# Optimization experiments

Measured on AMD Instinct MI355X. Metric: run time of the kernel, lower is better.

Reference implementation:

```python
import jax, jax.numpy as jnp
import numpy as np

K, D, N, T, B = 8, 16, 32, 200, 2048
_LOG2PI = float(np.log(2.0 * np.pi))


def setup_inputs() -> dict:
    key = jax.random.key(0)
    ks = jax.random.split(key, 13)
    return {
        "discrete_states": jax.random.randint(ks[0], (B, T), 0, K),
        "continuous_states": jax.random.normal(ks[1], (B, T, D), dtype=jnp.float32),
        "obs": jax.random.normal(ks[2], (B, T, N), dtype=jnp.float32),
        "discrete_init_logits": jax.random.normal(ks[3], (K,), dtype=jnp.float32),
        "continuous_init_locs": jax.random.normal(ks[4], (K, D), dtype=jnp.float32),
        "continuous_init_log_scales": jax.random.normal(ks[5], (K, D), dtype=jnp.float32),
        "state_transition_logits": jax.random.normal(ks[6], (K, K), dtype=jnp.float32),
        "dynamics_matrices": jax.random.normal(ks[7], (K, D, D), dtype=jnp.float32) * 0.3,
        "dynamics_offsets": jax.random.normal(ks[8], (K, D), dtype=jnp.float32),
        # NOTE: original code uses dynamics_log_scales directly as a scale (missing .exp());
        # we keep that math faithfully but init it strictly positive to stay finite.
        "dynamics_log_scales": jax.random.uniform(ks[9], (K, D), minval=0.5, maxval=1.5, dtype=jnp.float32),
        "emission_matrices": jax.random.normal(ks[10], (K, N, D), dtype=jnp.float32),
        "emission_offsets": jax.random.normal(ks[11], (K, N), dtype=jnp.float32),
        "emission_log_scales": jax.random.normal(ks[12], (K, N), dtype=jnp.float32),
    }


def _normal_lp(x, loc, scale):
    # elementwise Normal log-prob
    return -0.5 * jnp.square((x - loc) / scale) - jnp.log(scale) - 0.5 * _LOG2PI


def reference(discrete_states, continuous_states, obs,
              discrete_init_logits, continuous_init_locs, continuous_init_log_scales,
              state_transition_logits, dynamics_matrices, dynamics_offsets,
              dynamics_log_scales, emission_matrices, emission_offsets,
              emission_log_scales):
    """log p(s_{1:T}, z_{1:T}, x_{1:T}) -> [B]"""
    s0 = discrete_states[:, 0]                      # [B]
    z0 = continuous_states[:, 0]                    # [B,D]
    # p(s_1)
    lp = jax.nn.log_softmax(discrete_init_logits)[s0]
    # p(z_1 | s_1)
    lp = lp + _normal_lp(z0, continuous_init_locs[s0],
                         jnp.exp(continuous_init_log_scales[s0])).sum(-1)
    # p(s_t | s_{t-1}) for t=2..T, fully vectorized over time
    s_prev = discrete_states[:, :-1]
    s_cur = discrete_states[:, 1:]
    trans = jax.nn.log_softmax(state_transition_logits, axis=-1)  # [K,K]
    lp = lp + trans[s_prev, s_cur].sum(-1)
    # p(z_t | z_{t-1}, s_t)
    A = dynamics_matrices[s_cur]                    # [B,T-1,D,D] gather
    dyn_loc = jnp.einsum('btij,btj->bti', A, continuous_states[:, :-1]) + dynamics_offsets[s_cur]
    dyn_scale = dynamics_log_scales[s_cur]          # faithful: original omits .exp()
    lp = lp + _normal_lp(continuous_states[:, 1:], dyn_loc, dyn_scale).sum((-1, -2))
    # p(x_t | z_t, s_t) for all t
    C = emission_matrices[discrete_states]          # [B,T,N,D] gather
    em_loc = jnp.einsum('btij,btj->bti', C, continuous_states) + emission_offsets[discrete_states]
    em_scale = jnp.exp(emission_log_scales[discrete_states])
    lp = lp + _normal_lp(obs, em_loc, em_scale).sum((-1, -2))
    return lp
```

## Files before the change

### kernel.cpp

```cpp
#include <hip/hip_runtime.h>

#define KK 8
#define DD 16
#define NN 32
#define TT 200
#define BB 2048

#define SCU 260
#define SAU 132
#define SE 36
#define SD 20

__device__ __forceinline__ float bflo(unsigned u) { return __uint_as_float(u << 16); }
__device__ __forceinline__ float bfhi(unsigned u) { return __uint_as_float(u & 0xffff0000u); }

__device__ __forceinline__ unsigned bfr(float f) {
  unsigned u = __float_as_uint(f);
  return (u + 0x7fffu + ((u >> 16) & 1u)) >> 16;
}
__device__ __forceinline__ unsigned bfpack(float f0, float f1) {
  return bfr(f0) | (bfr(f1) << 16);
}

__device__ __forceinline__ float dot16bf(const unsigned* __restrict__ row,
                                         const float* __restrict__ z) {
  uint4 w0 = *reinterpret_cast<const uint4*>(row);
  uint4 w1 = *reinterpret_cast<const uint4*>(row + 4);
  float a = bflo(w0.x) * z[0], b = bfhi(w0.x) * z[1];
  a = fmaf(bflo(w0.y), z[2], a);  b = fmaf(bfhi(w0.y), z[3], b);
  a = fmaf(bflo(w0.z), z[4], a);  b = fmaf(bfhi(w0.z), z[5], b);
  a = fmaf(bflo(w0.w), z[6], a);  b = fmaf(bfhi(w0.w), z[7], b);
  a = fmaf(bflo(w1.x), z[8], a);  b = fmaf(bfhi(w1.x), z[9], b);
  a = fmaf(bflo(w1.y), z[10], a); b = fmaf(bfhi(w1.y), z[11], b);
  a = fmaf(bflo(w1.z), z[12], a); b = fmaf(bfhi(w1.z), z[13], b);
  a = fmaf(bflo(w1.w), z[14], a); b = fmaf(bfhi(w1.w), z[15], b);
  return a + b;
}

__global__ __launch_bounds__(256) void slds_lp_kernel(
    const int* __restrict__ dsts,
    const float* __restrict__ zg,
    const float* __restrict__ obsg,
    const float* __restrict__ initlg,
    const float* __restrict__ initloc,
    const float* __restrict__ initls,
    const float* __restrict__ transg,
    const float* __restrict__ Ag,
    const float* __restrict__ dynoff,
    const float* __restrict__ dynls,
    const float* __restrict__ Cg,
    const float* __restrict__ emoff,
    const float* __restrict__ emls,
    float* __restrict__ out)
{
  __shared__ __align__(16) unsigned sCu[KK * SCU];
  __shared__ __align__(16) unsigned sAu[KK * SAU];
  __shared__ __align__(16) float sEmOff[KK * SE];
  __shared__ __align__(16) float sEmInv[KK * SE];
  __shared__ __align__(16) float sDynOff[KK * SD];
  __shared__ __align__(16) float sDynInv[KK * SD];
  __shared__ __align__(16) float sInitLoc[KK * SD];
  __shared__ __align__(16) float sInitInv[KK * SD];
  __shared__ float sTrans[KK * KK];
  __shared__ float sEmConst[KK];
  __shared__ float sDynConst[KK];
  __shared__ float sInitLp[KK];

  const float HALF_LOG2PI = 0.91893853320467274178f;
  const int tid = threadIdx.x;

  for (int i = tid; i < KK * NN * DD / 2; i += 256) {
    int k = i >> 8, r = i & 255;
    sCu[k * SCU + r] = bfpack(Cg[2 * i], Cg[2 * i + 1]);
  }
  for (int i = tid; i < KK * DD * DD / 2; i += 256) {
    int k = i >> 7, r = i & 127;
    sAu[k * SAU + r] = bfpack(Ag[2 * i], Ag[2 * i + 1]);
  }
  if (tid < KK * NN) {
    int k = tid >> 5, n = tid & 31;
    sEmOff[k * SE + n] = emoff[tid];
    sEmInv[k * SE + n] = expf(-emls[tid]);
  }
  if (tid < KK * DD) {
    int k = tid >> 4, d = tid & 15;
    sDynOff[k * SD + d] = dynoff[tid];
    sDynInv[k * SD + d] = 1.0f / dynls[tid];
    sInitLoc[k * SD + d] = initloc[tid];
    sInitInv[k * SD + d] = expf(-initls[tid]);
  }
  if (tid < KK * KK) {
    int kr = tid >> 3;
    float mx = transg[kr * KK];
    for (int j = 1; j < KK; ++j) mx = fmaxf(mx, transg[kr * KK + j]);
    float ss = 0.f;
    for (int j = 0; j < KK; ++j) ss += expf(transg[kr * KK + j] - mx);
    sTrans[tid] = transg[tid] - (logf(ss) + mx);
  }
  if (tid < KK) {
    int k = tid;
    float se = 0.f;
    for (int n = 0; n < NN; ++n) se -= emls[k * NN + n];
    sEmConst[k] = se - NN * HALF_LOG2PI;
    float sd = 0.f;
    for (int d = 0; d < DD; ++d) sd -= logf(dynls[k * DD + d]);
    sDynConst[k] = sd - DD * HALF_LOG2PI;
    float mx = initlg[0];
    for (int j = 1; j < KK; ++j) mx = fmaxf(mx, initlg[j]);
    float ss = 0.f;
    for (int j = 0; j < KK; ++j) ss += expf(initlg[j] - mx);
    float si = 0.f;
    for (int d = 0; d < DD; ++d) si -= initls[k * DD + d];
    sInitLp[k] = initlg[k] - (logf(ss) + mx) + si - DD * HALF_LOG2PI;
  }
  __syncthreads();

  const int nItems = BB * TT;
  const int gstride = gridDim.x * blockDim.x;
  for (int item = blockIdx.x * blockDim.x + tid; item < nItems; item += gstride) {
    const int b = item / TT;
    const int t = item - b * TT;

    float z[16];
    {
      const float4* p = reinterpret_cast<const float4*>(zg + (size_t)item * DD);
      float4 a0 = p[0], a1 = p[1], a2 = p[2], a3 = p[3];
      z[0] = a0.x; z[1] = a0.y; z[2] = a0.z; z[3] = a0.w;
      z[4] = a1.x; z[5] = a1.y; z[6] = a1.z; z[7] = a1.w;
      z[8] = a2.x; z[9] = a2.y; z[10] = a2.z; z[11] = a2.w;
      z[12] = a3.x; z[13] = a3.y; z[14] = a3.z; z[15] = a3.w;
    }
    const int s = dsts[item];

    const float4* o4 = reinterpret_cast<const float4*>(obsg + (size_t)item * NN);
    const int cb = s * SCU;
    const int eb4 = s * (SE / 4);
    float acc = 0.f;
#pragma unroll 2
    for (int g = 0; g < 8; ++g) {
      float4 o = o4[g];
      float4 off = reinterpret_cast<const float4*>(sEmOff)[eb4 + g];
      float4 inv = reinterpret_cast<const float4*>(sEmInv)[eb4 + g];
      int n0 = g * 4;
      float l0 = dot16bf(&sCu[cb + (n0 + 0) * 8], z) + off.x;
      float l1 = dot16bf(&sCu[cb + (n0 + 1) * 8], z) + off.y;
      float l2 = dot16bf(&sCu[cb + (n0 + 2) * 8], z) + off.z;
      float l3 = dot16bf(&sCu[cb + (n0 + 3) * 8], z) + off.w;
      float d0 = (o.x - l0) * inv.x;
      float d1 = (o.y - l1) * inv.y;
      float d2 = (o.z - l2) * inv.z;
      float d3 = (o.w - l3) * inv.w;
      acc = fmaf(d0, d0, acc); acc = fmaf(d1, d1, acc);
      acc = fmaf(d2, d2, acc); acc = fmaf(d3, d3, acc);
    }
    float lp = -0.5f * acc + sEmConst[s];

    if (t != 0) {
      const int sp = dsts[item - 1];
      float zp[16];
      {
        const float4* p = reinterpret_cast<const float4*>(zg + (size_t)(item - 1) * DD);
        float4 a0 = p[0], a1 = p[1], a2 = p[2], a3 = p[3];
        zp[0] = a0.x; zp[1] = a0.y; zp[2] = a0.z; zp[3] = a0.w;
        zp[4] = a1.x; zp[5] = a1.y; zp[6] = a1.z; zp[7] = a1.w;
        zp[8] = a2.x; zp[9] = a2.y; zp[10] = a2.z; zp[11] = a2.w;
        zp[12] = a3.x; zp[13] = a3.y; zp[14] = a3.z; zp[15] = a3.w;
      }
      const int ab = s * SAU;
      const int db4 = s * (SD / 4);
      float a2acc = 0.f;
#pragma unroll 2
      for (int g = 0; g < 4; ++g) {
        float4 off = reinterpret_cast<const float4*>(sDynOff)[db4 + g];
        float4 inv = reinterpret_cast<const float4*>(sDynInv)[db4 + g];
        int i0 = g * 4;
        float l0 = dot16bf(&sAu[ab + (i0 + 0) * 8], zp) + off.x;
        float l1 = dot16bf(&sAu[ab + (i0 + 1) * 8], zp) + off.y;
        float l2 = dot16bf(&sAu[ab + (i0 + 2) * 8], zp) + off.z;
        float l3 = dot16bf(&sAu[ab + (i0 + 3) * 8], zp) + off.w;
        float d0 = (z[i0 + 0] - l0) * inv.x;
        float d1 = (z[i0 + 1] - l1) * inv.y;
        float d2 = (z[i0 + 2] - l2) * inv.z;
        float d3 = (z[i0 + 3] - l3) * inv.w;
        a2acc = fmaf(d0, d0, a2acc); a2acc = fmaf(d1, d1, a2acc);
        a2acc = fmaf(d2, d2, a2acc); a2acc = fmaf(d3, d3, a2acc);
      }
      lp += -0.5f * a2acc + sDynConst[s] + sTrans[sp * KK + s];
    } else {
      const int ib4 = s * (SD / 4);
      float a2acc = 0.f;
#pragma unroll 2
      for (int g = 0; g < 4; ++g) {
        float4 loc = reinterpret_cast<const float4*>(sInitLoc)[ib4 + g];
        float4 inv = reinterpret_cast<const float4*>(sInitInv)[ib4 + g];
        int i0 = g * 4;
        float d0 = (z[i0 + 0] - loc.x) * inv.x;
        float d1 = (z[i0 + 1] - loc.y) * inv.y;
        float d2 = (z[i0 + 2] - loc.z) * inv.z;
        float d3 = (z[i0 + 3] - loc.w) * inv.w;
        a2acc = fmaf(d0, d0, a2acc); a2acc = fmaf(d1, d1, a2acc);
        a2acc = fmaf(d2, d2, a2acc); a2acc = fmaf(d3, d3, a2acc);
      }
      lp += -0.5f * a2acc + sInitLp[s];
    }

    const int lane = tid & 63;
    float v = lp;
#pragma unroll
    for (int off = 1; off < 64; off <<= 1) {
      float ov = __shfl_up(v, off, 64);
      int obk = __shfl_up(b, off, 64);
      if (lane >= off && obk == b) v += ov;
    }
    int nb = __shfl_down(b, 1, 64);
    if (lane == 63 || nb != b) atomicAdd(&out[b], v);
  }
}

extern "C" void kernel_launch(void* const* d_in, const int* in_sizes, int n_in,
                              void* d_out, int out_size, void* d_ws, size_t ws_size,
                              hipStream_t stream) {
  const int*   dsts    = (const int*)d_in[0];
  const float* zg      = (const float*)d_in[1];
  const float* obsg    = (const float*)d_in[2];
  const float* initlg  = (const float*)d_in[3];
  const float* initloc = (const float*)d_in[4];
  const float* initls  = (const float*)d_in[5];
  const float* transg  = (const float*)d_in[6];
  const float* Ag      = (const float*)d_in[7];
  const float* dynoff  = (const float*)d_in[8];
  const float* dynls   = (const float*)d_in[9];
  const float* Cg      = (const float*)d_in[10];
  const float* emoff   = (const float*)d_in[11];
  const float* emls    = (const float*)d_in[12];
  float* out = (float*)d_out;

  hipMemsetAsync(d_out, 0, BB * sizeof(float), stream);

  slds_lp_kernel<<<1600, 256, 0, stream>>>(dsts, zg, obsg, initlg, initloc,
                                           initls, transg, Ag, dynoff, dynls,
                                           Cg, emoff, emls, out);
}
```

Baseline: 147.4 us.

## Precompute parameter tables in prep kernel and shuffle previous z across lanes

Adds a single-block prep kernel that packs the C and A matrices to bf16, computes the log-softmax and scale constants, and zeroes the output, all written to workspace. The main kernel then only copies these tables into shared memory, so each of the 1600 blocks no longer repeats the conversion and transcendental math. The previous time step's z and discrete state now come from the neighbouring lane by warp shuffle, with only lane 0 reading global memory, which halves the z loads. The cost is one extra small kernel launch in front of the main one and 16 extra shuffles per item.

```diff
diff --git a/kernel.cpp b/kernel.cpp
--- a/kernel.cpp
+++ b/kernel.cpp
@@ -10,6 +10,19 @@
 #define SAU 132
 #define SE 36
 #define SD 20
+
+#define WS_CU    0
+#define WS_AU    2048
+#define WS_EMOFF 3072
+#define WS_EMINV 3328
+#define WS_DYOFF 3584
+#define WS_DYINV 3712
+#define WS_INLOC 3840
+#define WS_ININV 3968
+#define WS_TRANS 4096
+#define WS_EMC   4160
+#define WS_DYC   4168
+#define WS_INLP  4176
 
 __device__ __forceinline__ float bflo(unsigned u) { return __uint_as_float(u << 16); }
 __device__ __forceinline__ float bfhi(unsigned u) { return __uint_as_float(u & 0xffff0000u); }
@@ -37,20 +50,60 @@
   return a + b;
 }
 
+__global__ __launch_bounds__(256) void prep_kernel(
+    const float* __restrict__ initlg, const float* __restrict__ initloc,
+    const float* __restrict__ initls, const float* __restrict__ transg,
+    const float* __restrict__ Ag, const float* __restrict__ dynoff,
+    const float* __restrict__ dynls, const float* __restrict__ Cg,
+    const float* __restrict__ emoff, const float* __restrict__ emls,
+    unsigned* __restrict__ ws, float* __restrict__ out) {
+  const float HALF_LOG2PI = 0.91893853320467274178f;
+  const int tid = threadIdx.x;
+  float* wsf = reinterpret_cast<float*>(ws);
+
+  for (int i = tid; i < 2048; i += 256)
+    ws[WS_CU + i] = bfpack(Cg[2 * i], Cg[2 * i + 1]);
+  for (int i = tid; i < 1024; i += 256)
+    ws[WS_AU + i] = bfpack(Ag[2 * i], Ag[2 * i + 1]);
+  if (tid < 256) { wsf[WS_EMOFF + tid] = emoff[tid]; wsf[WS_EMINV + tid] = expf(-emls[tid]); }
+  if (tid < 128) {
+    wsf[WS_DYOFF + tid] = dynoff[tid];
+    wsf[WS_DYINV + tid] = 1.0f / dynls[tid];
+    wsf[WS_INLOC + tid] = initloc[tid];
+    wsf[WS_ININV + tid] = expf(-initls[tid]);
+  }
+  if (tid < 64) {
+    int kr = tid >> 3;
+    float mx = transg[kr * KK];
+    for (int j = 1; j < KK; ++j) mx = fmaxf(mx, transg[kr * KK + j]);
+    float ss = 0.f;
+    for (int j = 0; j < KK; ++j) ss += expf(transg[kr * KK + j] - mx);
+    wsf[WS_TRANS + tid] = transg[tid] - (logf(ss) + mx);
+  }
+  if (tid < 8) {
+    int k = tid;
+    float se = 0.f;
+    for (int n = 0; n < NN; ++n) se -= emls[k * NN + n];
+    wsf[WS_EMC + k] = se - NN * HALF_LOG2PI;
+    float sd = 0.f;
+    for (int d = 0; d < DD; ++d) sd -= logf(dynls[k * DD + d]);
+    wsf[WS_DYC + k] = sd - DD * HALF_LOG2PI;
+    float mx = initlg[0];
+    for (int j = 1; j < KK; ++j) mx = fmaxf(mx, initlg[j]);
+    float ss = 0.f;
+    for (int j = 0; j < KK; ++j) ss += expf(initlg[j] - mx);
+    float si = 0.f;
+    for (int d = 0; d < DD; ++d) si -= initls[k * DD + d];
+    wsf[WS_INLP + k] = initlg[k] - (logf(ss) + mx) + si - DD * HALF_LOG2PI;
+  }
+  for (int i = tid; i < BB; i += 256) out[i] = 0.f;
+}
+
 __global__ __launch_bounds__(256) void slds_lp_kernel(
     const int* __restrict__ dsts,
     const float* __restrict__ zg,
     const float* __restrict__ obsg,
-    const float* __restrict__ initlg,
-    const float* __restrict__ initloc,
-    const float* __restrict__ initls,
-    const float* __restrict__ transg,
-    const float* __restrict__ Ag,
-    const float* __restrict__ dynoff,
-    const float* __restrict__ dynls,
-    const float* __restrict__ Cg,
-    const float* __restrict__ emoff,
-    const float* __restrict__ emls,
+    const unsigned* __restrict__ ws,
     float* __restrict__ out)
 {
   __shared__ __align__(16) unsigned sCu[KK * SCU];
@@ -66,52 +119,34 @@
   __shared__ float sDynConst[KK];
   __shared__ float sInitLp[KK];
 
-  const float HALF_LOG2PI = 0.91893853320467274178f;
   const int tid = threadIdx.x;
-
-  for (int i = tid; i < KK * NN * DD / 2; i += 256) {
+  const float* wsf = reinterpret_cast<const float*>(ws);
+
+  for (int i = tid; i < 2048; i += 256) {
     int k = i >> 8, r = i & 255;
-    sCu[k * SCU + r] = bfpack(Cg[2 * i], Cg[2 * i + 1]);
-  }
-  for (int i = tid; i < KK * DD * DD / 2; i += 256) {
+    sCu[k * SCU + r] = ws[WS_CU + i];
+  }
+  for (int i = tid; i < 1024; i += 256) {
     int k = i >> 7, r = i & 127;
-    sAu[k * SAU + r] = bfpack(Ag[2 * i], Ag[2 * i + 1]);
-  }
-  if (tid < KK * NN) {
+    sAu[k * SAU + r] = ws[WS_AU + i];
+  }
+  if (tid < 256) {
     int k = tid >> 5, n = tid & 31;
-    sEmOff[k * SE + n] = emoff[tid];
-    sEmInv[k * SE + n] = expf(-emls[tid]);
-  }
-  if (tid < KK * DD) {
+    sEmOff[k * SE + n] = wsf[WS_EMOFF + tid];
+    sEmInv[k * SE + n] = wsf[WS_EMINV + tid];
+  }
+  if (tid < 128) {
     int k = tid >> 4, d = tid & 15;
-    sDynOff[k * SD + d] = dynoff[tid];
-    sDynInv[k * SD + d] = 1.0f / dynls[tid];
-    sInitLoc[k * SD + d] = initloc[tid];
-    sInitInv[k * SD + d] = expf(-initls[tid]);
-  }
-  if (tid < KK * KK) {
-    int kr = tid >> 3;
-    float mx = transg[kr * KK];
-    for (int j = 1; j < KK; ++j) mx = fmaxf(mx, transg[kr * KK + j]);
-    float ss = 0.f;
-    for (int j = 0; j < KK; ++j) ss += expf(transg[kr * KK + j] - mx);
-    sTrans[tid] = transg[tid] - (logf(ss) + mx);
-  }
-  if (tid < KK) {
-    int k = tid;
-    float se = 0.f;
-    for (int n = 0; n < NN; ++n) se -= emls[k * NN + n];
-    sEmConst[k] = se - NN * HALF_LOG2PI;
-    float sd = 0.f;
-    for (int d = 0; d < DD; ++d) sd -= logf(dynls[k * DD + d]);
-    sDynConst[k] = sd - DD * HALF_LOG2PI;
-    float mx = initlg[0];
-    for (int j = 1; j < KK; ++j) mx = fmaxf(mx, initlg[j]);
-    float ss = 0.f;
-    for (int j = 0; j < KK; ++j) ss += expf(initlg[j] - mx);
-    float si = 0.f;
-    for (int d = 0; d < DD; ++d) si -= initls[k * DD + d];
-    sInitLp[k] = initlg[k] - (logf(ss) + mx) + si - DD * HALF_LOG2PI;
+    sDynOff[k * SD + d] = wsf[WS_DYOFF + tid];
+    sDynInv[k * SD + d] = wsf[WS_DYINV + tid];
+    sInitLoc[k * SD + d] = wsf[WS_INLOC + tid];
+    sInitInv[k * SD + d] = wsf[WS_ININV + tid];
+  }
+  if (tid < 64) sTrans[tid] = wsf[WS_TRANS + tid];
+  if (tid < 8) {
+    sEmConst[tid] = wsf[WS_EMC + tid];
+    sDynConst[tid] = wsf[WS_DYC + tid];
+    sInitLp[tid] = wsf[WS_INLP + tid];
   }
   __syncthreads();
 
@@ -120,17 +155,37 @@
   for (int item = blockIdx.x * blockDim.x + tid; item < nItems; item += gstride) {
     const int b = item / TT;
     const int t = item - b * TT;
-
-    float z[16];
+    const int lane = tid & 63;
+
+    float zz[16];
     {
       const float4* p = reinterpret_cast<const float4*>(zg + (size_t)item * DD);
       float4 a0 = p[0], a1 = p[1], a2 = p[2], a3 = p[3];
-      z[0] = a0.x; z[1] = a0.y; z[2] = a0.z; z[3] = a0.w;
-      z[4] = a1.x; z[5] = a1.y; z[6] = a1.z; z[7] = a1.w;
-      z[8] = a2.x; z[9] = a2.y; z[10] = a2.z; z[11] = a2.w;
-      z[12] = a3.x; z[13] = a3.y; z[14] = a3.z; z[15] = a3.w;
+      zz[0] = a0.x; zz[1] = a0.y; zz[2] = a0.z; zz[3] = a0.w;
+      zz[4] = a1.x; zz[5] = a1.y; zz[6] = a1.z; zz[7] = a1.w;
+      zz[8] = a2.x; zz[9] = a2.y; zz[10] = a2.z; zz[11] = a2.w;
+      zz[12] = a3.x; zz[13] = a3.y; zz[14] = a3.z; zz[15] = a3.w;
     }
     const int s = dsts[item];
+
+    float zpg[4];
+    float zp[16];
+    int sp = __shfl_up(s, 1, 64);
+    if (lane == 0 && t != 0) {
+      sp = dsts[item - 1];
+      const float4* p = reinterpret_cast<const float4*>(zg + (size_t)(item - 1) * DD);
+      float4 a0 = p[0], a1 = p[1], a2 = p[2], a3 = p[3];
+      zp[0] = a0.x; zp[1] = a0.y; zp[2] = a0.z; zp[3] = a0.w;
+      zp[4] = a1.x; zp[5] = a1.y; zp[6] = a1.z; zp[7] = a1.w;
+      zp[8] = a2.x; zp[9] = a2.y; zp[10] = a2.z; zp[11] = a2.w;
+      zp[12] = a3.x; zp[13] = a3.y; zp[14] = a3.z; zp[15] = a3.w;
+    }
+#pragma unroll
+    for (int i = 0; i < 16; ++i) {
+      float sh = __shfl_up(zz[i], 1, 64);
+      if (lane != 0) zp[i] = sh;
+    }
+    (void)zpg;
 
     const float4* o4 = reinterpret_cast<const float4*>(obsg + (size_t)item * NN);
     const int cb = s * SCU;
@@ -142,10 +197,10 @@
       float4 off = reinterpret_cast<const float4*>(sEmOff)[eb4 + g];
       float4 inv = reinterpret_cast<const float4*>(sEmInv)[eb4 + g];
       int n0 = g * 4;
-      float l0 = dot16bf(&sCu[cb + (n0 + 0) * 8], z) + off.x;
-      float l1 = dot16bf(&sCu[cb + (n0 + 1) * 8], z) + off.y;
-      float l2 = dot16bf(&sCu[cb + (n0 + 2) * 8], z) + off.z;
-      float l3 = dot16bf(&sCu[cb + (n0 + 3) * 8], z) + off.w;
+      float l0 = dot16bf(&sCu[cb + (n0 + 0) * 8], zz) + off.x;
+      float l1 = dot16bf(&sCu[cb + (n0 + 1) * 8], zz) + off.y;
+      float l2 = dot16bf(&sCu[cb + (n0 + 2) * 8], zz) + off.z;
+      float l3 = dot16bf(&sCu[cb + (n0 + 3) * 8], zz) + off.w;
       float d0 = (o.x - l0) * inv.x;
       float d1 = (o.y - l1) * inv.y;
       float d2 = (o.z - l2) * inv.z;
@@ -156,16 +211,6 @@
     float lp = -0.5f * acc + sEmConst[s];
 
     if (t != 0) {
-      const int sp = dsts[item - 1];
-      float zp[16];
-      {
-        const float4* p = reinterpret_cast<const float4*>(zg + (size_t)(item - 1) * DD);
-        float4 a0 = p[0], a1 = p[1], a2 = p[2], a3 = p[3];
-        zp[0] = a0.x; zp[1] = a0.y; zp[2] = a0.z; zp[3] = a0.w;
-        zp[4] = a1.x; zp[5] = a1.y; zp[6] = a1.z; zp[7] = a1.w;
-        zp[8] = a2.x; zp[9] = a2.y; zp[10] = a2.z; zp[11] = a2.w;
-        zp[12] = a3.x; zp[13] = a3.y; zp[14] = a3.z; zp[15] = a3.w;
-      }
       const int ab = s * SAU;
       const int db4 = s * (SD / 4);
       float a2acc = 0.f;
@@ -178,10 +223,10 @@
         float l1 = dot16bf(&sAu[ab + (i0 + 1) * 8], zp) + off.y;
         float l2 = dot16bf(&sAu[ab + (i0 + 2) * 8], zp) + off.z;
         float l3 = dot16bf(&sAu[ab + (i0 + 3) * 8], zp) + off.w;
-        float d0 = (z[i0 + 0] - l0) * inv.x;
-        float d1 = (z[i0 + 1] - l1) * inv.y;
-        float d2 = (z[i0 + 2] - l2) * inv.z;
-        float d3 = (z[i0 + 3] - l3) * inv.w;
+        float d0 = (zz[i0 + 0] - l0) * inv.x;
+        float d1 = (zz[i0 + 1] - l1) * inv.y;
+        float d2 = (zz[i0 + 2] - l2) * inv.z;
+        float d3 = (zz[i0 + 3] - l3) * inv.w;
         a2acc = fmaf(d0, d0, a2acc); a2acc = fmaf(d1, d1, a2acc);
         a2acc = fmaf(d2, d2, a2acc); a2acc = fmaf(d3, d3, a2acc);
       }
@@ -194,17 +239,16 @@
         float4 loc = reinterpret_cast<const float4*>(sInitLoc)[ib4 + g];
         float4 inv = reinterpret_cast<const float4*>(sInitInv)[ib4 + g];
         int i0 = g * 4;
-        float d0 = (z[i0 + 0] - loc.x) * inv.x;
-        float d1 = (z[i0 + 1] - loc.y) * inv.y;
-        float d2 = (z[i0 + 2] - loc.z) * inv.z;
-        float d3 = (z[i0 + 3] - loc.w) * inv.w;
+        float d0 = (zz[i0 + 0] - loc.x) * inv.x;
+        float d1 = (zz[i0 + 1] - loc.y) * inv.y;
+        float d2 = (zz[i0 + 2] - loc.z) * inv.z;
+        float d3 = (zz[i0 + 3] - loc.w) * inv.w;
         a2acc = fmaf(d0, d0, a2acc); a2acc = fmaf(d1, d1, a2acc);
         a2acc = fmaf(d2, d2, a2acc); a2acc = fmaf(d3, d3, a2acc);
       }
       lp += -0.5f * a2acc + sInitLp[s];
     }
 
-    const int lane = tid & 63;
     float v = lp;
 #pragma unroll
     for (int off = 1; off < 64; off <<= 1) {
@@ -234,10 +278,9 @@
   const float* emoff   = (const float*)d_in[11];
   const float* emls    = (const float*)d_in[12];
   float* out = (float*)d_out;
-
-  hipMemsetAsync(d_out, 0, BB * sizeof(float), stream);
-
-  slds_lp_kernel<<<1600, 256, 0, stream>>>(dsts, zg, obsg, initlg, initloc,
-                                           initls, transg, Ag, dynoff, dynls,
-                                           Cg, emoff, emls, out);
-}
+  unsigned* ws = (unsigned*)d_ws;
+
+  prep_kernel<<<1, 256, 0, stream>>>(initlg, initloc, initls, transg, Ag,
+                                     dynoff, dynls, Cg, emoff, emls, ws, out);
+  slds_lp_kernel<<<1600, 256, 0, stream>>>(dsts, zg, obsg, ws, out);
+}
```

Result: no change. 144.8 us (-1.8%).
